# Performance work log

Hardware: AMD Instinct MI355X
Metric: run time of the kernel (lower is better)

## Reference

```python
import jax, jax.numpy as jnp
import numpy as np

ROI = 7
NMS_THR = 0.01
NMS_SIZE = 100


def crop_and_resize(fmap, boxes, crop):
    # fmap [H,W,C], boxes [N,4] normalized (y1,x1,y2,x2) -> [N,crop,crop,C]
    H, W, C = fmap.shape
    t = jnp.linspace(0.0, 1.0, crop)
    ys = (boxes[:, 0:1] + (boxes[:, 2:3] - boxes[:, 0:1]) * t) * (H - 1)  # [N,crop]
    xs = (boxes[:, 1:2] + (boxes[:, 3:4] - boxes[:, 1:2]) * t) * (W - 1)
    y0 = jnp.clip(jnp.floor(ys), 0, H - 1).astype(jnp.int32)
    x0 = jnp.clip(jnp.floor(xs), 0, W - 1).astype(jnp.int32)
    y1 = jnp.clip(y0 + 1, 0, H - 1)
    x1 = jnp.clip(x0 + 1, 0, W - 1)
    wy = (ys - y0)[:, :, None, None]
    wx = (xs - x0)[:, None, :, None]
    Y0, Y1 = y0[:, :, None], y1[:, :, None]
    X0, X1 = x0[:, None, :], x1[:, None, :]
    f00 = fmap[Y0, X0]; f01 = fmap[Y0, X1]
    f10 = fmap[Y1, X0]; f11 = fmap[Y1, X1]
    return (f00 * (1 - wy) * (1 - wx) + f01 * (1 - wy) * wx
            + f10 * wy * (1 - wx) + f11 * wy * wx)


def iou_matrix(b):
    # b [N,4] (x1,y1,x2,y2)
    area = jnp.maximum(b[:, 2] - b[:, 0], 0) * jnp.maximum(b[:, 3] - b[:, 1], 0)
    lt = jnp.maximum(b[:, None, :2], b[None, :, :2])
    rb = jnp.minimum(b[:, None, 2:], b[None, :, 2:])
    wh = jnp.maximum(rb - lt, 0.0)
    inter = wh[..., 0] * wh[..., 1]
    return inter / (area[:, None] + area[None, :] - inter + 1e-8)


def nms(boxes, scores, thr, max_out):
    # greedy NMS, fixed-size output (pads with lowest-ranked boxes when fewer survive)
    N = boxes.shape[0]
    order = jnp.argsort(-scores)
    M = iou_matrix(boxes[order])
    idx = jnp.arange(N)
    def body(i, keep):
        sup = (M[i] > thr) & (idx > i) & keep[i]
        return keep & ~sup
    keep = jax.lax.fori_loop(0, N, body, jnp.ones(N, dtype=bool))
    rank = jnp.where(keep, idx, N + idx)
    sel = jnp.argsort(rank)[:max_out]
    return order[sel]


def make_boxes(key, n):
    kc, ks = jax.random.split(key)
    c = jax.random.uniform(kc, (n, 2), minval=0.1, maxval=0.9)
    s = jax.random.uniform(ks, (n, 2), minval=0.02, maxval=0.15)
    lo = jnp.clip(c - s / 2, 0.0, 1.0)
    hi = jnp.clip(c + s / 2, 0.0, 1.0)
    return jnp.concatenate([lo, hi], axis=1)  # (y1,x1,y2,x2)


def setup_inputs() -> dict:
    key = jax.random.key(0)
    ks = jax.random.split(key, 12)
    N, D, Hd = 1024, ROI * ROI * 32, 2048
    img_boxes = make_boxes(ks[0], N)
    bev_boxes = make_boxes(ks[1], N)
    bev_boxes_abs = bev_boxes[:, jnp.array([1, 0, 3, 2])] * 80.0  # (x1,y1,x2,y2) in meters
    def w(k, shape, fan_in):
        return jax.random.normal(k, shape, jnp.float32) * (2.0 / fan_in) ** 0.5
    return {
        'img_feat_map': jax.random.uniform(ks[2], (1, 360, 1200, 32), jnp.float32),
        'bev_feat_map': jax.random.uniform(ks[3], (1, 700, 800, 32), jnp.float32),
        'img_boxes': img_boxes,
        'bev_boxes': bev_boxes,
        'bev_boxes_abs': bev_boxes_abs,
        'img_mask': jnp.ones((1, 1, 1, 1), jnp.float32),
        'bev_mask': jnp.ones((1, 1, 1, 1), jnp.float32),
        'W1': w(ks[4], (D, Hd), D), 'b1': jnp.zeros((Hd,), jnp.float32),
        'W2': w(ks[5], (Hd, Hd), Hd), 'b2': jnp.zeros((Hd,), jnp.float32),
        'Wc': w(ks[6], (Hd, 2), Hd), 'bc': jnp.zeros((2,), jnp.float32),
        'Wo': w(ks[7], (Hd, 10), Hd), 'bo': jnp.zeros((10,), jnp.float32),
        'Wa': w(ks[8], (Hd, 2), Hd), 'ba': jnp.zeros((2,), jnp.float32),
    }


def reference(img_feat_map, bev_feat_map, img_boxes, bev_boxes, bev_boxes_abs,
              img_mask, bev_mask, W1, b1, W2, b2, Wc, bc, Wo, bo, Wa, ba):
    # ROI align on masked feature maps
    rois_rgb = crop_and_resize((img_mask * img_feat_map)[0], img_boxes, ROI)
    rois_bev = crop_and_resize((bev_mask * bev_feat_map)[0], bev_boxes, ROI)
    # mean fusion
    fused = (rois_rgb + rois_bev) / (img_mask + bev_mask)  # [N,7,7,32]
    # predictor
    x = fused.reshape(fused.shape[0], -1)
    h = jax.nn.relu(x @ W1 + b1)
    h = jax.nn.relu(h @ W2 + b2)
    obj = h @ Wc + bc            # [N,2]
    off = h @ Wo + bo            # [N,10]
    ang = h @ Wa + ba            # [N,2]
    obj_soft = jax.nn.softmax(obj, axis=1)
    orient = jnp.arctan2(ang[:, 1], ang[:, 0])  # convert_angle_to_orientation
    # offset-adjusted BEV boxes for NMS
    pb = bev_boxes_abs + 0.1 * off[:, :4]
    boxes = jnp.stack([jnp.minimum(pb[:, 0], pb[:, 2]), jnp.minimum(pb[:, 1], pb[:, 3]),
                       jnp.maximum(pb[:, 0], pb[:, 2]), jnp.maximum(pb[:, 1], pb[:, 3])], axis=1)
    scores = jnp.max(obj[:, 1:], axis=1)
    ti = nms(jax.lax.stop_gradient(boxes), jax.lax.stop_gradient(scores), NMS_THR, NMS_SIZE)
    # [100, 2 + 4 + 1]: softmax scores, pred bev boxes, orientations
    return jnp.concatenate([obj_soft[ti], boxes[ti], orient[ti][:, None]], axis=1)
```

## Files before the change

### kernel.cpp

```cpp
#include <hip/hip_runtime.h>
#include <math.h>

#define NBOX 1024
#define ROI_N 7
#define CH 32
#define FEAT (ROI_N*ROI_N*CH)
#define K1PAD 1664
#define HD 2048
#define NMS_THR_F 0.01f
#define NMS_OUT 100
#define MTRI_WORDS 8704

typedef _Float16 f16;
typedef f16 f16x8 __attribute__((ext_vector_type(8)));
typedef float f32x4 __attribute__((ext_vector_type(4)));

__device__ __forceinline__ void split_f16(float v, f16& h, f16& l) {
  h = (f16)v;
  l = (f16)((v - (float)h) * 4096.0f);
}

__global__ __launch_bounds__(256) void roi_fuse_kernel(
    const float* __restrict__ img, const float* __restrict__ bev,
    const float* __restrict__ img_boxes, const float* __restrict__ bev_boxes,
    const float* __restrict__ img_mask, const float* __restrict__ bev_mask,
    f16* __restrict__ xh, f16* __restrict__ xl)
{
  const int b = blockIdx.x;
  const float mi = img_mask[0], mb = bev_mask[0];
  const float denom = mi + mb;

  const float iy0 = img_boxes[b*4+0], ix0 = img_boxes[b*4+1];
  const float iy1 = img_boxes[b*4+2], ix1 = img_boxes[b*4+3];
  const float by0 = bev_boxes[b*4+0], bx0 = bev_boxes[b*4+1];
  const float by1 = bev_boxes[b*4+2], bx1 = bev_boxes[b*4+3];

  for (int idx = threadIdx.x; idx < K1PAD; idx += 256) {
    if (idx >= FEAT) {
      xh[(size_t)b*K1PAD + idx] = (f16)0.0f;
      xl[(size_t)b*K1PAD + idx] = (f16)0.0f;
      continue;
    }
    const int ti  = idx / (ROI_N*CH);
    const int rem = idx - ti*(ROI_N*CH);
    const int tj  = rem >> 5;
    const int c   = rem & 31;
    const float tt_i = (ti == ROI_N-1) ? 1.0f : ti * (1.0f/(ROI_N-1));
    const float tt_j = (tj == ROI_N-1) ? 1.0f : tj * (1.0f/(ROI_N-1));

    float vi, vb;
    {
      const int H = 360, W = 1200;
      const float ys = (iy0 + (iy1 - iy0) * tt_i) * (float)(H-1);
      const float xs = (ix0 + (ix1 - ix0) * tt_j) * (float)(W-1);
      int y0 = (int)floorf(ys); y0 = y0 < 0 ? 0 : (y0 > H-1 ? H-1 : y0);
      int x0 = (int)floorf(xs); x0 = x0 < 0 ? 0 : (x0 > W-1 ? W-1 : x0);
      const int y1 = (y0+1 > H-1) ? H-1 : y0+1;
      const int x1 = (x0+1 > W-1) ? W-1 : x0+1;
      const float wy = ys - (float)y0;
      const float wx = xs - (float)x0;
      const float f00 = img[(y0*W + x0)*CH + c];
      const float f01 = img[(y0*W + x1)*CH + c];
      const float f10 = img[(y1*W + x0)*CH + c];
      const float f11 = img[(y1*W + x1)*CH + c];
      vi = f00*(1.0f-wy)*(1.0f-wx) + f01*(1.0f-wy)*wx
         + f10*wy*(1.0f-wx)        + f11*wy*wx;
    }
    {
      const int H = 700, W = 800;
      const float ys = (by0 + (by1 - by0) * tt_i) * (float)(H-1);
      const float xs = (bx0 + (bx1 - bx0) * tt_j) * (float)(W-1);
      int y0 = (int)floorf(ys); y0 = y0 < 0 ? 0 : (y0 > H-1 ? H-1 : y0);
      int x0 = (int)floorf(xs); x0 = x0 < 0 ? 0 : (x0 > W-1 ? W-1 : x0);
      const int y1 = (y0+1 > H-1) ? H-1 : y0+1;
      const int x1 = (x0+1 > W-1) ? W-1 : x0+1;
      const float wy = ys - (float)y0;
      const float wx = xs - (float)x0;
      const float f00 = bev[(y0*W + x0)*CH + c];
      const float f01 = bev[(y0*W + x1)*CH + c];
      const float f10 = bev[(y1*W + x0)*CH + c];
      const float f11 = bev[(y1*W + x1)*CH + c];
      vb = f00*(1.0f-wy)*(1.0f-wx) + f01*(1.0f-wy)*wx
         + f10*wy*(1.0f-wx)        + f11*wy*wx;
    }
    f16 h, l;
    split_f16((mi*vi + mb*vb) / denom, h, l);
    xh[(size_t)b*K1PAD + idx] = h;
    xl[(size_t)b*K1PAD + idx] = l;
  }
}

__global__ __launch_bounds__(256) void convt_w_kernel(
    const float* __restrict__ W, f16* __restrict__ Wt_hi, f16* __restrict__ Wt_lo,
    int K, int Kpad, int N)
{
  __shared__ float t[64][33];
  const int tid = threadIdx.x;
  const int n0 = blockIdx.x * 32, k0 = blockIdx.y * 64;
#pragma unroll
  for (int p = 0; p < 8; ++p) {
    const int idx = tid + p*256;
    const int kk = idx >> 5, nn = idx & 31;
    const int k = k0 + kk;
    t[kk][nn] = (k < K) ? W[(size_t)k*N + n0 + nn] : 0.0f;
  }
  __syncthreads();
  const int nn = tid >> 3;
  const int kg = (tid & 7) * 8;
  f16x8 h8, l8;
#pragma unroll
  for (int q = 0; q < 8; ++q) {
    const float v = t[kg + q][nn];
    f16 h, l;
    split_f16(v, h, l);
    h8[q] = h; l8[q] = l;
  }
  *(f16x8*)&Wt_hi[(size_t)(n0+nn)*Kpad + k0 + kg] = h8;
  *(f16x8*)&Wt_lo[(size_t)(n0+nn)*Kpad + k0 + kg] = l8;
}

__global__ __launch_bounds__(256) void init_bias_kernel(
    const float* __restrict__ b1, const float* __restrict__ b2,
    float4* __restrict__ h1f, float4* __restrict__ h2f)
{
  const int idx = blockIdx.x*256 + threadIdx.x;
  const int c4 = idx & (HD/4 - 1);
  h1f[idx] = *(const float4*)&b1[c4*4];
  h2f[idx] = *(const float4*)&b2[c4*4];
}

#define STAGE_LOAD(KK)                                                          \
  do {                                                                          \
    _Pragma("unroll")                                                           \
    for (int q_ = 0; q_ < 2; ++q_) {                                            \
      const int ch_ = tid + q_*256;                                             \
      const int r_ = ch_ >> 2, c_ = (ch_ & 3) * 8;                              \
      if constexpr (AF32) {                                                     \
        paf[q_][0] = *(const float4*)&Af_g[(size_t)(m0 + r_)*K + (KK) + c_];    \
        paf[q_][1] = *(const float4*)&Af_g[(size_t)(m0 + r_)*K + (KK) + c_ + 4];\
      } else {                                                                  \
        pah[q_] = *(const f16x8*)&Ah_g[(size_t)(m0 + r_)*K + (KK) + c_];        \
        pal[q_] = *(const f16x8*)&Al_g[(size_t)(m0 + r_)*K + (KK) + c_];        \
      }                                                                         \
      pbh[q_] = *(const f16x8*)&Bh_g[(size_t)(n0 + r_)*K + (KK) + c_];          \
      pbl[q_] = *(const f16x8*)&Bl_g[(size_t)(n0 + r_)*K + (KK) + c_];          \
    }                                                                           \
  } while (0)

template<int AF32>
__global__ __launch_bounds__(256, 2) void gemm_sk(
    const f16* __restrict__ Ah_g, const f16* __restrict__ Al_g,
    const float* __restrict__ Af_g,
    const f16* __restrict__ Bh_g, const f16* __restrict__ Bl_g,
    float* __restrict__ Cout, int M, int N, int K, int kchunk)
{
  __shared__ f16 Ah[128][32], Al[128][32], Bh[128][32], Bl[128][32];
  const int tid = threadIdx.x;

  const int g = blockIdx.x;
  const int xcd = g & 7, c = g >> 3;
  const int nb = xcd*2 + (c & 1);
  const int mb = (c >> 1) & 7;
  const int zb = c >> 4;
  const int m0 = mb * 128, n0 = nb * 128;
  const int kb = zb * kchunk, ke = kb + kchunk;

  const int wid = tid >> 6, lane = tid & 63;
  const int wr = wid >> 1, wc = wid & 1;
  const int frow = lane & 15, fkg = lane >> 4;
  const int swz = (fkg ^ ((frow >> 1) & 3)) * 8;

  f32x4 acc1[4][4], acc2[4][4];
#pragma unroll
  for (int i = 0; i < 4; ++i)
#pragma unroll
    for (int j = 0; j < 4; ++j)
#pragma unroll
      for (int r = 0; r < 4; ++r) { acc1[i][j][r] = 0.0f; acc2[i][j][r] = 0.0f; }

  f16x8 pah[2], pal[2], pbh[2], pbl[2];
  float4 paf[2][2];

  STAGE_LOAD(kb);
  for (int kk = kb; kk < ke; kk += 32) {
    __syncthreads();
#pragma unroll
    for (int q = 0; q < 2; ++q) {
      const int ch = tid + q*256;
      const int r = ch >> 2, cs = ch & 3;
      const int sl = (cs ^ ((r >> 1) & 3)) * 8;
      if constexpr (AF32) {
        const float4 a0 = paf[q][0], a1 = paf[q][1];
        f16x8 hv, lv;
        { float v = fmaxf(a0.x, 0.0f); f16 h,l; split_f16(v,h,l); hv[0]=h; lv[0]=l; }
        { float v = fmaxf(a0.y, 0.0f); f16 h,l; split_f16(v,h,l); hv[1]=h; lv[1]=l; }
        { float v = fmaxf(a0.z, 0.0f); f16 h,l; split_f16(v,h,l); hv[2]=h; lv[2]=l; }
        { float v = fmaxf(a0.w, 0.0f); f16 h,l; split_f16(v,h,l); hv[3]=h; lv[3]=l; }
        { float v = fmaxf(a1.x, 0.0f); f16 h,l; split_f16(v,h,l); hv[4]=h; lv[4]=l; }
        { float v = fmaxf(a1.y, 0.0f); f16 h,l; split_f16(v,h,l); hv[5]=h; lv[5]=l; }
        { float v = fmaxf(a1.z, 0.0f); f16 h,l; split_f16(v,h,l); hv[6]=h; lv[6]=l; }
        { float v = fmaxf(a1.w, 0.0f); f16 h,l; split_f16(v,h,l); hv[7]=h; lv[7]=l; }
        *(f16x8*)&Ah[r][sl] = hv;
        *(f16x8*)&Al[r][sl] = lv;
      } else {
        *(f16x8*)&Ah[r][sl] = pah[q];
        *(f16x8*)&Al[r][sl] = pal[q];
      }
      *(f16x8*)&Bh[r][sl] = pbh[q];
      *(f16x8*)&Bl[r][sl] = pbl[q];
    }
    __syncthreads();
    if (kk + 32 < ke) { STAGE_LOAD(kk + 32); }

    f16x8 bh[4], bl[4];
#pragma unroll
    for (int j = 0; j < 4; ++j) {
      const int rr = wc*64 + j*16 + frow;
      bh[j] = *(const f16x8*)&Bh[rr][swz];
      bl[j] = *(const f16x8*)&Bl[rr][swz];
    }
#pragma unroll
    for (int i = 0; i < 4; ++i) {
      const int rr = wr*64 + i*16 + frow;
      const f16x8 ah = *(const f16x8*)&Ah[rr][swz];
      const f16x8 al = *(const f16x8*)&Al[rr][swz];
#pragma unroll
      for (int j = 0; j < 4; ++j) {
        acc1[i][j] = __builtin_amdgcn_mfma_f32_16x16x32_f16(ah, bh[j], acc1[i][j], 0, 0, 0);
        acc2[i][j] = __builtin_amdgcn_mfma_f32_16x16x32_f16(ah, bl[j], acc2[i][j], 0, 0, 0);
        acc2[i][j] = __builtin_amdgcn_mfma_f32_16x16x32_f16(al, bh[j], acc2[i][j], 0, 0, 0);
      }
    }
  }

  const float s = 1.0f / 4096.0f;
#pragma unroll
  for (int i = 0; i < 4; ++i)
#pragma unroll
    for (int j = 0; j < 4; ++j) {
      const int col = n0 + wc*64 + j*16 + frow;
#pragma unroll
      for (int r = 0; r < 4; ++r) {
        const int row = m0 + wr*64 + i*16 + fkg*4 + r;
        atomicAdd(&Cout[(size_t)row*N + col], acc1[i][j][r] + acc2[i][j][r] * s);
      }
    }
}

__global__ __launch_bounds__(256) void heads_kernel(
    const float* __restrict__ h2f,
    const float* __restrict__ Wc, const float* __restrict__ bc,
    const float* __restrict__ Wo, const float* __restrict__ bo,
    const float* __restrict__ Wa, const float* __restrict__ ba,
    const float* __restrict__ bev_abs,
    float* __restrict__ obj_soft, float* __restrict__ boxes,
    float* __restrict__ orient, float* __restrict__ scores)
{
  const int r = blockIdx.x;
  const int tid = threadIdx.x;
  float acc[14];
#pragma unroll
  for (int j = 0; j < 14; ++j) acc[j] = 0.0f;
  for (int k = tid; k < HD; k += 256) {
    const float hv = fmaxf(h2f[(size_t)r*HD + k], 0.0f);
    acc[0]  += hv * Wc[k*2+0];
    acc[1]  += hv * Wc[k*2+1];
#pragma unroll
    for (int j = 0; j < 10; ++j) acc[2+j] += hv * Wo[k*10+j];
    acc[12] += hv * Wa[k*2+0];
    acc[13] += hv * Wa[k*2+1];
  }
  __shared__ float red[14][256];
#pragma unroll
  for (int j = 0; j < 14; ++j) red[j][tid] = acc[j];
  __syncthreads();
  for (int s = 128; s > 0; s >>= 1) {
    if (tid < s) {
#pragma unroll
      for (int j = 0; j < 14; ++j) red[j][tid] += red[j][tid + s];
    }
    __syncthreads();
  }
  if (tid == 0) {
    const float obj0 = red[0][0] + bc[0];
    const float obj1 = red[1][0] + bc[1];
    float off0 = red[2][0] + bo[0];
    float off1 = red[3][0] + bo[1];
    float off2 = red[4][0] + bo[2];
    float off3 = red[5][0] + bo[3];
    const float a0 = red[12][0] + ba[0];
    const float a1 = red[13][0] + ba[1];

    const float m  = fmaxf(obj0, obj1);
    const float e0 = expf(obj0 - m), e1 = expf(obj1 - m);
    const float se = e0 + e1;
    obj_soft[r*2+0] = e0 / se;
    obj_soft[r*2+1] = e1 / se;
    orient[r] = atan2f(a1, a0);

    const float pb0 = bev_abs[r*4+0] + 0.1f*off0;
    const float pb1 = bev_abs[r*4+1] + 0.1f*off1;
    const float pb2 = bev_abs[r*4+2] + 0.1f*off2;
    const float pb3 = bev_abs[r*4+3] + 0.1f*off3;
    boxes[r*4+0] = fminf(pb0, pb2);
    boxes[r*4+1] = fminf(pb1, pb3);
    boxes[r*4+2] = fmaxf(pb0, pb2);
    boxes[r*4+3] = fmaxf(pb1, pb3);
    scores[r] = obj1;
  }
}

__global__ __launch_bounds__(128) void sort_kernel(
    const float* __restrict__ scores, const float* __restrict__ boxes,
    int* __restrict__ order, float4* __restrict__ sboxes, float* __restrict__ sarea)
{
  const int i = blockIdx.x * 128 + threadIdx.x;
  const float my = scores[i];
  int pos = 0;
  for (int j = 0; j < NBOX; ++j) {
    const float sj = scores[j];
    pos += (sj > my) || (sj == my && j < i);
  }
  const float b0 = boxes[i*4+0], b1 = boxes[i*4+1];
  const float b2 = boxes[i*4+2], b3 = boxes[i*4+3];
  order[pos]  = i;
  sboxes[pos] = make_float4(b0, b1, b2, b3);
  sarea[pos]  = fmaxf(b2 - b0, 0.0f) * fmaxf(b3 - b1, 0.0f);
}

__device__ __forceinline__ int tri_base(int i) {
  const int b = i >> 6;
  return 64*(16*b - (b*(b-1))/2) + (i & 63)*(16 - b);
}

__global__ __launch_bounds__(256) void maskbuild_kernel(
    const float4* __restrict__ sboxes, const float* __restrict__ sarea,
    unsigned long long* __restrict__ Mtri)
{
  __shared__ float4 sb[NBOX];
  __shared__ float  sa[NBOX];
  const int tid = threadIdx.x;
  for (int t = tid; t < NBOX; t += 256) { sb[t] = sboxes[t]; sa[t] = sarea[t]; }
  __syncthreads();
  const int wv = tid >> 6, lane = tid & 63;
  for (int r = 0; r < 4; ++r) {
    const int i = blockIdx.x * 16 + wv * 4 + r;
    const float4 bi = sb[i];
    const float  ai = sa[i];
    const int b = i >> 6;
    const int base = tri_base(i);
    for (int w = b; w < 16; ++w) {
      const int j = w * 64 + lane;
      const float4 bj = sb[j];
      const float lt0 = fmaxf(bi.x, bj.x), lt1 = fmaxf(bi.y, bj.y);
      const float rb0 = fminf(bi.z, bj.z), rb1 = fminf(bi.w, bj.w);
      const float wq = fmaxf(rb0 - lt0, 0.0f), hq = fmaxf(rb1 - lt1, 0.0f);
      const float inter = wq * hq;
      const float iou = inter / (ai + sa[j] - inter + 1e-8f);
      const unsigned long long bits = __ballot((j > i) && (iou > NMS_THR_F));
      if (lane == 0) Mtri[base + (w - b)] = bits;
    }
  }
}

__global__ __launch_bounds__(1024) void scan_out_kernel(
    const unsigned long long* __restrict__ Mtri_g, const int* __restrict__ order,
    const float4* __restrict__ sboxes, const float* __restrict__ obj_soft,
    const float* __restrict__ orient, float* __restrict__ out)
{
  __shared__ unsigned long long M[MTRI_WORDS];
  __shared__ unsigned long long keepw[16];
  const int tid = threadIdx.x;
  for (int t = tid; t < MTRI_WORDS; t += 1024) M[t] = Mtri_g[t];
  __syncthreads();

  if (tid < 64) {
    const int lane = tid;
    unsigned long long kw = (lane < 16) ? ~0ull : 0ull;
    for (int w = 0; w < 16; ++w) {
      unsigned long long rem = __shfl(kw, w);
      while (rem) {
        const int bpos = __builtin_ctzll(rem);
        const int i = w * 64 + bpos;
        const int base = tri_base(i);
        unsigned long long m = 0;
        if (lane >= w && lane < 16) m = M[base + (lane - w)];
        kw &= ~m;
        const unsigned long long updated = __shfl(kw, w);
        rem = (bpos == 63) ? 0ull : (updated & (~0ull << (bpos + 1)));
      }
    }
    if (lane < 16) keepw[lane] = kw;
  }
  __syncthreads();

  const int w = tid >> 6, bpos = tid & 63;
  int pre = 0, total = 0;
#pragma unroll
  for (int q = 0; q < 16; ++q) {
    const int pc = __popcll(keepw[q]);
    total += pc;
    if (q < w) pre += pc;
  }
  pre += __popcll(keepw[w] & ((bpos == 0) ? 0ull : (~0ull >> (64 - bpos))));
  const int keep_self = (int)((keepw[w] >> bpos) & 1ull);
  const int rank = keep_self ? pre : (total + tid - pre);

  if (rank < NMS_OUT) {
    const int ob = order[tid];
    const float4 bx = sboxes[tid];
    out[rank*7+0] = obj_soft[ob*2+0];
    out[rank*7+1] = obj_soft[ob*2+1];
    out[rank*7+2] = bx.x;
    out[rank*7+3] = bx.y;
    out[rank*7+4] = bx.z;
    out[rank*7+5] = bx.w;
    out[rank*7+6] = orient[ob];
  }
}

extern "C" void kernel_launch(void* const* d_in, const int* in_sizes, int n_in,
                              void* d_out, int out_size, void* d_ws, size_t ws_size,
                              hipStream_t stream) {
  (void)in_sizes; (void)n_in; (void)out_size; (void)ws_size;
  const float* img       = (const float*)d_in[0];
  const float* bev       = (const float*)d_in[1];
  const float* img_boxes = (const float*)d_in[2];
  const float* bev_boxes = (const float*)d_in[3];
  const float* bev_abs   = (const float*)d_in[4];
  const float* img_mask  = (const float*)d_in[5];
  const float* bev_mask  = (const float*)d_in[6];
  const float* W1 = (const float*)d_in[7];
  const float* b1 = (const float*)d_in[8];
  const float* W2 = (const float*)d_in[9];
  const float* b2 = (const float*)d_in[10];
  const float* Wc = (const float*)d_in[11];
  const float* bc = (const float*)d_in[12];
  const float* Wo = (const float*)d_in[13];
  const float* bo = (const float*)d_in[14];
  const float* Wa = (const float*)d_in[15];
  const float* ba = (const float*)d_in[16];
  float* out = (float*)d_out;

  char* ws = (char*)d_ws;
  f16* xh    = (f16*)ws;                                  ws += (size_t)NBOX*K1PAD*2;
  f16* xl    = (f16*)ws;                                  ws += (size_t)NBOX*K1PAD*2;
  float* h1f = (float*)ws;                                ws += (size_t)NBOX*HD*4;
  float* h2f = (float*)ws;                                ws += (size_t)NBOX*HD*4;
  f16* Wt1h  = (f16*)ws;                                  ws += (size_t)HD*K1PAD*2;
  f16* Wt1l  = (f16*)ws;                                  ws += (size_t)HD*K1PAD*2;
  f16* Wt2h  = (f16*)ws;                                  ws += (size_t)HD*HD*2;
  f16* Wt2l  = (f16*)ws;                                  ws += (size_t)HD*HD*2;
  float* obj_soft = (float*)ws;                           ws += NBOX*2*4;
  float* boxesf   = (float*)ws;                           ws += NBOX*4*4;
  float* orient   = (float*)ws;                           ws += NBOX*4;
  float* scores   = (float*)ws;                           ws += NBOX*4;
  int*   order    = (int*)ws;                             ws += NBOX*4;
  float4* sboxes  = (float4*)ws;                          ws += NBOX*16;
  float* sarea    = (float*)ws;                           ws += NBOX*4;
  unsigned long long* Mtri = (unsigned long long*)ws;

  roi_fuse_kernel<<<NBOX, 256, 0, stream>>>(img, bev, img_boxes, bev_boxes,
                                            img_mask, bev_mask, xh, xl);
  init_bias_kernel<<<NBOX*HD/4/256, 256, 0, stream>>>(b1, b2, (float4*)h1f, (float4*)h2f);
  convt_w_kernel<<<dim3(HD/32, K1PAD/64), 256, 0, stream>>>(W1, Wt1h, Wt1l, FEAT, K1PAD, HD);
  convt_w_kernel<<<dim3(HD/32, HD/64),    256, 0, stream>>>(W2, Wt2h, Wt2l, HD, HD, HD);
  gemm_sk<0><<<512, 256, 0, stream>>>(xh, xl, (const float*)nullptr,
                                      Wt1h, Wt1l, h1f, NBOX, HD, K1PAD, K1PAD/4);
  gemm_sk<1><<<512, 256, 0, stream>>>((const f16*)nullptr, (const f16*)nullptr, h1f,
                                      Wt2h, Wt2l, h2f, NBOX, HD, HD, HD/4);
  heads_kernel<<<NBOX, 256, 0, stream>>>(h2f, Wc, bc, Wo, bo, Wa, ba, bev_abs,
                                         obj_soft, boxesf, orient, scores);
  sort_kernel<<<8, 128, 0, stream>>>(scores, boxesf, order, sboxes, sarea);
  maskbuild_kernel<<<64, 256, 0, stream>>>(sboxes, sarea, Mtri);
  scan_out_kernel<<<1, 1024, 0, stream>>>(Mtri, order, sboxes, obj_soft, orient, out);
}
```

Measured before the change: 370.3 us.

## Merge prep kernels, vectorize ROI gather, use direct global-to-LDS loads in GEMM

Folds the ROI crop/fuse, both weight transpose-splits and the bias init into one prep kernel, cutting launch count. The ROI gather now reads float4 vectors, with each thread handling eight channels. The GEMM drops its register-staged prefetch and instead has each wave issue global_load_lds 16-byte copies straight into swizzled LDS. A separate split_relu kernel pre-splits the layer-1 output into f16 hi/lo halves, so the second GEMM no longer converts fp32 inline. The trade-offs are an extra launch and extra workspace traffic, and loss of the software prefetch overlap in the GEMM main loop.

```diff
diff --git a/kernel.cpp b/kernel.cpp
--- a/kernel.cpp
+++ b/kernel.cpp
@@ -12,6 +12,7 @@
 #define MTRI_WORDS 8704
 
 typedef _Float16 f16;
+typedef f16 f16x4 __attribute__((ext_vector_type(4)));
 typedef f16 f16x8 __attribute__((ext_vector_type(8)));
 typedef float f32x4 __attribute__((ext_vector_type(4)));
 
@@ -20,89 +21,145 @@
   l = (f16)((v - (float)h) * 4096.0f);
 }
 
-__global__ __launch_bounds__(256) void roi_fuse_kernel(
+__device__ __forceinline__ void gload_lds16(const void* g, void* l) {
+  __builtin_amdgcn_global_load_lds(
+      (const __attribute__((address_space(1))) unsigned int*)g,
+      (__attribute__((address_space(3))) unsigned int*)l, 16, 0, 0);
+}
+
+#define B_ROI 1024
+#define B_C1  (64*26)
+#define B_C2  (64*32)
+#define B_INIT 2048
+
+__device__ void roi_part(int b, int tid,
+    const float* __restrict__ img, const float* __restrict__ bev,
+    const float* __restrict__ img_boxes, const float* __restrict__ bev_boxes,
+    float mi, float mb, f16* __restrict__ xh, f16* __restrict__ xl)
+{
+  const float denom = mi + mb;
+  if (tid >= 196) {
+    const int g = tid - 196;
+    if (g < 12) {
+      f16x8 z = {};
+      *(f16x8*)&xh[(size_t)b*K1PAD + FEAT + g*8] = z;
+      *(f16x8*)&xl[(size_t)b*K1PAD + FEAT + g*8] = z;
+    }
+    return;
+  }
+  const int cell = tid >> 2, cg = (tid & 3) * 8;
+  const int ti = cell / ROI_N, tj = cell - ti*ROI_N;
+  const float tt_i = (ti == 6) ? 1.0f : ti * (1.0f/6.0f);
+  const float tt_j = (tj == 6) ? 1.0f : tj * (1.0f/6.0f);
+
+  float vi[8], vb[8];
+  {
+    const int H = 360, W = 1200;
+    const float iy0 = img_boxes[b*4+0], ix0 = img_boxes[b*4+1];
+    const float iy1 = img_boxes[b*4+2], ix1 = img_boxes[b*4+3];
+    const float ys = (iy0 + (iy1 - iy0) * tt_i) * (float)(H-1);
+    const float xs = (ix0 + (ix1 - ix0) * tt_j) * (float)(W-1);
+    int y0 = (int)floorf(ys); y0 = y0 < 0 ? 0 : (y0 > H-1 ? H-1 : y0);
+    int x0 = (int)floorf(xs); x0 = x0 < 0 ? 0 : (x0 > W-1 ? W-1 : x0);
+    const int y1 = (y0+1 > H-1) ? H-1 : y0+1;
+    const int x1 = (x0+1 > W-1) ? W-1 : x0+1;
+    const float wy = ys - (float)y0, wx = xs - (float)x0;
+    const float w00 = (1.0f-wy)*(1.0f-wx), w01 = (1.0f-wy)*wx;
+    const float w10 = wy*(1.0f-wx),        w11 = wy*wx;
+    const float* p00 = &img[(y0*W + x0)*CH + cg];
+    const float* p01 = &img[(y0*W + x1)*CH + cg];
+    const float* p10 = &img[(y1*W + x0)*CH + cg];
+    const float* p11 = &img[(y1*W + x1)*CH + cg];
+#pragma unroll
+    for (int q = 0; q < 2; ++q) {
+      const float4 f00 = *(const float4*)(p00 + q*4);
+      const float4 f01 = *(const float4*)(p01 + q*4);
+      const float4 f10 = *(const float4*)(p10 + q*4);
+      const float4 f11 = *(const float4*)(p11 + q*4);
+      vi[q*4+0] = f00.x*w00 + f01.x*w01 + f10.x*w10 + f11.x*w11;
+      vi[q*4+1] = f00.y*w00 + f01.y*w01 + f10.y*w10 + f11.y*w11;
+      vi[q*4+2] = f00.z*w00 + f01.z*w01 + f10.z*w10 + f11.z*w11;
+      vi[q*4+3] = f00.w*w00 + f01.w*w01 + f10.w*w10 + f11.w*w11;
+    }
+  }
+  {
+    const int H = 700, W = 800;
+    const float by0 = bev_boxes[b*4+0], bx0 = bev_boxes[b*4+1];
+    const float by1 = bev_boxes[b*4+2], bx1 = bev_boxes[b*4+3];
+    const float ys = (by0 + (by1 - by0) * tt_i) * (float)(H-1);
+    const float xs = (bx0 + (bx1 - bx0) * tt_j) * (float)(W-1);
+    int y0 = (int)floorf(ys); y0 = y0 < 0 ? 0 : (y0 > H-1 ? H-1 : y0);
+    int x0 = (int)floorf(xs); x0 = x0 < 0 ? 0 : (x0 > W-1 ? W-1 : x0);
+    const int y1 = (y0+1 > H-1) ? H-1 : y0+1;
+    const int x1 = (x0+1 > W-1) ? W-1 : x0+1;
+    const float wy = ys - (float)y0, wx = xs - (float)x0;
+    const float w00 = (1.0f-wy)*(1.0f-wx), w01 = (1.0f-wy)*wx;
+    const float w10 = wy*(1.0f-wx),        w11 = wy*wx;
+    const float* p00 = &bev[(y0*W + x0)*CH + cg];
+    const float* p01 = &bev[(y0*W + x1)*CH + cg];
+    const float* p10 = &bev[(y1*W + x0)*CH + cg];
+    const float* p11 = &bev[(y1*W + x1)*CH + cg];
+#pragma unroll
+    for (int q = 0; q < 2; ++q) {
+      const float4 f00 = *(const float4*)(p00 + q*4);
+      const float4 f01 = *(const float4*)(p01 + q*4);
+      const float4 f10 = *(const float4*)(p10 + q*4);
+      const float4 f11 = *(const float4*)(p11 + q*4);
+      vb[q*4+0] = f00.x*w00 + f01.x*w01 + f10.x*w10 + f11.x*w11;
+      vb[q*4+1] = f00.y*w00 + f01.y*w01 + f10.y*w10 + f11.y*w11;
+      vb[q*4+2] = f00.z*w00 + f01.z*w01 + f10.z*w10 + f11.z*w11;
+      vb[q*4+3] = f00.w*w00 + f01.w*w01 + f10.w*w10 + f11.w*w11;
+    }
+  }
+  f16x8 h8, l8;
+#pragma unroll
+  for (int q = 0; q < 8; ++q) {
+    f16 h, l;
+    split_f16((mi*vi[q] + mb*vb[q]) / denom, h, l);
+    h8[q] = h; l8[q] = l;
+  }
+  const size_t o = (size_t)b*K1PAD + cell*32 + cg;
+  *(f16x8*)&xh[o] = h8;
+  *(f16x8*)&xl[o] = l8;
+}
+
+__global__ __launch_bounds__(256) void prep_kernel(
     const float* __restrict__ img, const float* __restrict__ bev,
     const float* __restrict__ img_boxes, const float* __restrict__ bev_boxes,
     const float* __restrict__ img_mask, const float* __restrict__ bev_mask,
-    f16* __restrict__ xh, f16* __restrict__ xl)
-{
-  const int b = blockIdx.x;
-  const float mi = img_mask[0], mb = bev_mask[0];
-  const float denom = mi + mb;
-
-  const float iy0 = img_boxes[b*4+0], ix0 = img_boxes[b*4+1];
-  const float iy1 = img_boxes[b*4+2], ix1 = img_boxes[b*4+3];
-  const float by0 = bev_boxes[b*4+0], bx0 = bev_boxes[b*4+1];
-  const float by1 = bev_boxes[b*4+2], bx1 = bev_boxes[b*4+3];
-
-  for (int idx = threadIdx.x; idx < K1PAD; idx += 256) {
-    if (idx >= FEAT) {
-      xh[(size_t)b*K1PAD + idx] = (f16)0.0f;
-      xl[(size_t)b*K1PAD + idx] = (f16)0.0f;
-      continue;
-    }
-    const int ti  = idx / (ROI_N*CH);
-    const int rem = idx - ti*(ROI_N*CH);
-    const int tj  = rem >> 5;
-    const int c   = rem & 31;
-    const float tt_i = (ti == ROI_N-1) ? 1.0f : ti * (1.0f/(ROI_N-1));
-    const float tt_j = (tj == ROI_N-1) ? 1.0f : tj * (1.0f/(ROI_N-1));
-
-    float vi, vb;
-    {
-      const int H = 360, W = 1200;
-      const float ys = (iy0 + (iy1 - iy0) * tt_i) * (float)(H-1);
-      const float xs = (ix0 + (ix1 - ix0) * tt_j) * (float)(W-1);
-      int y0 = (int)floorf(ys); y0 = y0 < 0 ? 0 : (y0 > H-1 ? H-1 : y0);
-      int x0 = (int)floorf(xs); x0 = x0 < 0 ? 0 : (x0 > W-1 ? W-1 : x0);
-      const int y1 = (y0+1 > H-1) ? H-1 : y0+1;
-      const int x1 = (x0+1 > W-1) ? W-1 : x0+1;
-      const float wy = ys - (float)y0;
-      const float wx = xs - (float)x0;
-      const float f00 = img[(y0*W + x0)*CH + c];
-      const float f01 = img[(y0*W + x1)*CH + c];
-      const float f10 = img[(y1*W + x0)*CH + c];
-      const float f11 = img[(y1*W + x1)*CH + c];
-      vi = f00*(1.0f-wy)*(1.0f-wx) + f01*(1.0f-wy)*wx
-         + f10*wy*(1.0f-wx)        + f11*wy*wx;
-    }
-    {
-      const int H = 700, W = 800;
-      const float ys = (by0 + (by1 - by0) * tt_i) * (float)(H-1);
-      const float xs = (bx0 + (bx1 - bx0) * tt_j) * (float)(W-1);
-      int y0 = (int)floorf(ys); y0 = y0 < 0 ? 0 : (y0 > H-1 ? H-1 : y0);
-      int x0 = (int)floorf(xs); x0 = x0 < 0 ? 0 : (x0 > W-1 ? W-1 : x0);
-      const int y1 = (y0+1 > H-1) ? H-1 : y0+1;
-      const int x1 = (x0+1 > W-1) ? W-1 : x0+1;
-      const float wy = ys - (float)y0;
-      const float wx = xs - (float)x0;
-      const float f00 = bev[(y0*W + x0)*CH + c];
-      const float f01 = bev[(y0*W + x1)*CH + c];
-      const float f10 = bev[(y1*W + x0)*CH + c];
-      const float f11 = bev[(y1*W + x1)*CH + c];
-      vb = f00*(1.0f-wy)*(1.0f-wx) + f01*(1.0f-wy)*wx
-         + f10*wy*(1.0f-wx)        + f11*wy*wx;
-    }
-    f16 h, l;
-    split_f16((mi*vi + mb*vb) / denom, h, l);
-    xh[(size_t)b*K1PAD + idx] = h;
-    xl[(size_t)b*K1PAD + idx] = l;
-  }
-}
-
-__global__ __launch_bounds__(256) void convt_w_kernel(
-    const float* __restrict__ W, f16* __restrict__ Wt_hi, f16* __restrict__ Wt_lo,
-    int K, int Kpad, int N)
+    f16* __restrict__ xh, f16* __restrict__ xl,
+    const float* __restrict__ W1, f16* __restrict__ Wt1h, f16* __restrict__ Wt1l,
+    const float* __restrict__ W2, f16* __restrict__ Wt2h, f16* __restrict__ Wt2l,
+    const float* __restrict__ b1, const float* __restrict__ b2,
+    float4* __restrict__ h1f, float4* __restrict__ h2f)
 {
   __shared__ float t[64][33];
+  const int g = blockIdx.x;
   const int tid = threadIdx.x;
-  const int n0 = blockIdx.x * 32, k0 = blockIdx.y * 64;
+
+  if (g < B_ROI) {
+    roi_part(g, tid, img, bev, img_boxes, bev_boxes, img_mask[0], bev_mask[0], xh, xl);
+    return;
+  }
+  const float* W; f16 *Wh, *Wl; int K, Kpad, cb;
+  if (g < B_ROI + B_C1) { cb = g - B_ROI;        W = W1; Wh = Wt1h; Wl = Wt1l; K = FEAT; Kpad = K1PAD; }
+  else if (g < B_ROI + B_C1 + B_C2) { cb = g - B_ROI - B_C1; W = W2; Wh = Wt2h; Wl = Wt2l; K = HD; Kpad = HD; }
+  else {
+    const int ib = g - B_ROI - B_C1 - B_C2;
+    const int idx = ib*256 + tid;
+    const int c4 = idx & (HD/4 - 1);
+    h1f[idx] = *(const float4*)&b1[c4*4];
+    h2f[idx] = *(const float4*)&b2[c4*4];
+    return;
+  }
+  const int nt = cb & 63, kt = cb >> 6;
+  const int n0 = nt * 32, k0 = kt * 64;
 #pragma unroll
   for (int p = 0; p < 8; ++p) {
     const int idx = tid + p*256;
     const int kk = idx >> 5, nn = idx & 31;
     const int k = k0 + kk;
-    t[kk][nn] = (k < K) ? W[(size_t)k*N + n0 + nn] : 0.0f;
+    t[kk][nn] = (k < K) ? W[(size_t)k*HD + n0 + nn] : 0.0f;
   }
   __syncthreads();
   const int nn = tid >> 3;
@@ -110,51 +167,34 @@
   f16x8 h8, l8;
 #pragma unroll
   for (int q = 0; q < 8; ++q) {
-    const float v = t[kg + q][nn];
     f16 h, l;
-    split_f16(v, h, l);
+    split_f16(t[kg + q][nn], h, l);
     h8[q] = h; l8[q] = l;
   }
-  *(f16x8*)&Wt_hi[(size_t)(n0+nn)*Kpad + k0 + kg] = h8;
-  *(f16x8*)&Wt_lo[(size_t)(n0+nn)*Kpad + k0 + kg] = l8;
-}
-
-__global__ __launch_bounds__(256) void init_bias_kernel(
-    const float* __restrict__ b1, const float* __restrict__ b2,
-    float4* __restrict__ h1f, float4* __restrict__ h2f)
+  *(f16x8*)&Wh[(size_t)(n0+nn)*Kpad + k0 + kg] = h8;
+  *(f16x8*)&Wl[(size_t)(n0+nn)*Kpad + k0 + kg] = l8;
+}
+
+__global__ __launch_bounds__(256) void split_relu_kernel(
+    const float* __restrict__ in, f16* __restrict__ oh, f16* __restrict__ ol)
 {
   const int idx = blockIdx.x*256 + threadIdx.x;
-  const int c4 = idx & (HD/4 - 1);
-  h1f[idx] = *(const float4*)&b1[c4*4];
-  h2f[idx] = *(const float4*)&b2[c4*4];
-}
-
-#define STAGE_LOAD(KK)                                                          \
-  do {                                                                          \
-    _Pragma("unroll")                                                           \
-    for (int q_ = 0; q_ < 2; ++q_) {                                            \
-      const int ch_ = tid + q_*256;                                             \
-      const int r_ = ch_ >> 2, c_ = (ch_ & 3) * 8;                              \
-      if constexpr (AF32) {                                                     \
-        paf[q_][0] = *(const float4*)&Af_g[(size_t)(m0 + r_)*K + (KK) + c_];    \
-        paf[q_][1] = *(const float4*)&Af_g[(size_t)(m0 + r_)*K + (KK) + c_ + 4];\
-      } else {                                                                  \
-        pah[q_] = *(const f16x8*)&Ah_g[(size_t)(m0 + r_)*K + (KK) + c_];        \
-        pal[q_] = *(const f16x8*)&Al_g[(size_t)(m0 + r_)*K + (KK) + c_];        \
-      }                                                                         \
-      pbh[q_] = *(const f16x8*)&Bh_g[(size_t)(n0 + r_)*K + (KK) + c_];          \
-      pbl[q_] = *(const f16x8*)&Bl_g[(size_t)(n0 + r_)*K + (KK) + c_];          \
-    }                                                                           \
-  } while (0)
-
-template<int AF32>
+  const float4 v = *(const float4*)&in[idx*4];
+  f16x4 h4, l4;
+  { f16 h,l; split_f16(fmaxf(v.x,0.0f),h,l); h4[0]=h; l4[0]=l; }
+  { f16 h,l; split_f16(fmaxf(v.y,0.0f),h,l); h4[1]=h; l4[1]=l; }
+  { f16 h,l; split_f16(fmaxf(v.z,0.0f),h,l); h4[2]=h; l4[2]=l; }
+  { f16 h,l; split_f16(fmaxf(v.w,0.0f),h,l); h4[3]=h; l4[3]=l; }
+  *(f16x4*)&oh[idx*4] = h4;
+  *(f16x4*)&ol[idx*4] = l4;
+}
+
 __global__ __launch_bounds__(256, 2) void gemm_sk(
     const f16* __restrict__ Ah_g, const f16* __restrict__ Al_g,
-    const float* __restrict__ Af_g,
     const f16* __restrict__ Bh_g, const f16* __restrict__ Bl_g,
     float* __restrict__ Cout, int M, int N, int K, int kchunk)
 {
-  __shared__ f16 Ah[128][32], Al[128][32], Bh[128][32], Bl[128][32];
+  __shared__ __align__(16) f16 Ah[128][32], Al[128][32], Bh[128][32], Bl[128][32];
   const int tid = threadIdx.x;
 
   const int g = blockIdx.x;
@@ -170,6 +210,13 @@
   const int frow = lane & 15, fkg = lane >> 4;
   const int swz = (fkg ^ ((frow >> 1) & 3)) * 8;
 
+  const f16* sarr; f16* larr; int rbase;
+  if (wid == 0)      { sarr = Ah_g; larr = &Ah[0][0]; rbase = m0; }
+  else if (wid == 1) { sarr = Al_g; larr = &Al[0][0]; rbase = m0; }
+  else if (wid == 2) { sarr = Bh_g; larr = &Bh[0][0]; rbase = n0; }
+  else               { sarr = Bl_g; larr = &Bl[0][0]; rbase = n0; }
+  const int lr = lane >> 2, lg = lane & 3;
+
   f32x4 acc1[4][4], acc2[4][4];
 #pragma unroll
   for (int i = 0; i < 4; ++i)
@@ -178,39 +225,15 @@
 #pragma unroll
       for (int r = 0; r < 4; ++r) { acc1[i][j][r] = 0.0f; acc2[i][j][r] = 0.0f; }
 
-  f16x8 pah[2], pal[2], pbh[2], pbl[2];
-  float4 paf[2][2];
-
-  STAGE_LOAD(kb);
   for (int kk = kb; kk < ke; kk += 32) {
     __syncthreads();
 #pragma unroll
-    for (int q = 0; q < 2; ++q) {
-      const int ch = tid + q*256;
-      const int r = ch >> 2, cs = ch & 3;
-      const int sl = (cs ^ ((r >> 1) & 3)) * 8;
-      if constexpr (AF32) {
-        const float4 a0 = paf[q][0], a1 = paf[q][1];
-        f16x8 hv, lv;
-        { float v = fmaxf(a0.x, 0.0f); f16 h,l; split_f16(v,h,l); hv[0]=h; lv[0]=l; }
-        { float v = fmaxf(a0.y, 0.0f); f16 h,l; split_f16(v,h,l); hv[1]=h; lv[1]=l; }
-        { float v = fmaxf(a0.z, 0.0f); f16 h,l; split_f16(v,h,l); hv[2]=h; lv[2]=l; }
-        { float v = fmaxf(a0.w, 0.0f); f16 h,l; split_f16(v,h,l); hv[3]=h; lv[3]=l; }
-        { float v = fmaxf(a1.x, 0.0f); f16 h,l; split_f16(v,h,l); hv[4]=h; lv[4]=l; }
-        { float v = fmaxf(a1.y, 0.0f); f16 h,l; split_f16(v,h,l); hv[5]=h; lv[5]=l; }
-        { float v = fmaxf(a1.z, 0.0f); f16 h,l; split_f16(v,h,l); hv[6]=h; lv[6]=l; }
-        { float v = fmaxf(a1.w, 0.0f); f16 h,l; split_f16(v,h,l); hv[7]=h; lv[7]=l; }
-        *(f16x8*)&Ah[r][sl] = hv;
-        *(f16x8*)&Al[r][sl] = lv;
-      } else {
-        *(f16x8*)&Ah[r][sl] = pah[q];
-        *(f16x8*)&Al[r][sl] = pal[q];
-      }
-      *(f16x8*)&Bh[r][sl] = pbh[q];
-      *(f16x8*)&Bl[r][sl] = pbl[q];
+    for (int q = 0; q < 8; ++q) {
+      const int r = q*16 + lr;
+      const int sg = lg ^ ((r >> 1) & 3);
+      gload_lds16(&sarr[(size_t)(rbase + r)*K + kk + sg*8], larr + q*512);
     }
     __syncthreads();
-    if (kk + 32 < ke) { STAGE_LOAD(kk + 32); }
 
     f16x8 bh[4], bl[4];
 #pragma unroll
@@ -446,6 +469,8 @@
   f16* xh    = (f16*)ws;                                  ws += (size_t)NBOX*K1PAD*2;
   f16* xl    = (f16*)ws;                                  ws += (size_t)NBOX*K1PAD*2;
   float* h1f = (float*)ws;                                ws += (size_t)NBOX*HD*4;
+  f16* h1h   = (f16*)ws;                                  ws += (size_t)NBOX*HD*2;
+  f16* h1l   = (f16*)ws;                                  ws += (size_t)NBOX*HD*2;
   float* h2f = (float*)ws;                                ws += (size_t)NBOX*HD*4;
   f16* Wt1h  = (f16*)ws;                                  ws += (size_t)HD*K1PAD*2;
   f16* Wt1l  = (f16*)ws;                                  ws += (size_t)HD*K1PAD*2;
@@ -460,15 +485,12 @@
   float* sarea    = (float*)ws;                           ws += NBOX*4;
   unsigned long long* Mtri = (unsigned long long*)ws;
 
-  roi_fuse_kernel<<<NBOX, 256, 0, stream>>>(img, bev, img_boxes, bev_boxes,
-                                            img_mask, bev_mask, xh, xl);
-  init_bias_kernel<<<NBOX*HD/4/256, 256, 0, stream>>>(b1, b2, (float4*)h1f, (float4*)h2f);
-  convt_w_kernel<<<dim3(HD/32, K1PAD/64), 256, 0, stream>>>(W1, Wt1h, Wt1l, FEAT, K1PAD, HD);
-  convt_w_kernel<<<dim3(HD/32, HD/64),    256, 0, stream>>>(W2, Wt2h, Wt2l, HD, HD, HD);
-  gemm_sk<0><<<512, 256, 0, stream>>>(xh, xl, (const float*)nullptr,
-                                      Wt1h, Wt1l, h1f, NBOX, HD, K1PAD, K1PAD/4);
-  gemm_sk<1><<<512, 256, 0, stream>>>((const f16*)nullptr, (const f16*)nullptr, h1f,
-                                      Wt2h, Wt2l, h2f, NBOX, HD, HD, HD/4);
+  prep_kernel<<<B_ROI + B_C1 + B_C2 + B_INIT, 256, 0, stream>>>(
+      img, bev, img_boxes, bev_boxes, img_mask, bev_mask, xh, xl,
+      W1, Wt1h, Wt1l, W2, Wt2h, Wt2l, b1, b2, (float4*)h1f, (float4*)h2f);
+  gemm_sk<<<512, 256, 0, stream>>>(xh, xl, Wt1h, Wt1l, h1f, NBOX, HD, K1PAD, K1PAD/4);
+  split_relu_kernel<<<NBOX*HD/4/256, 256, 0, stream>>>(h1f, h1h, h1l);
+  gemm_sk<<<512, 256, 0, stream>>>(h1h, h1l, Wt2h, Wt2l, h2f, NBOX, HD, HD, HD/4);
   heads_kernel<<<NBOX, 256, 0, stream>>>(h2f, Wc, bc, Wo, bo, Wa, ba, bev_abs,
                                          obj_soft, boxesf, orient, scores);
   sort_kernel<<<8, 128, 0, stream>>>(scores, boxesf, order, sboxes, sarea);
```

New measurement: 359.2 us. -3.0%, faster.
